# Performance work log

Measured on AMD Instinct MI355X. Metric: run time of the kernel, lower is better.

Reference implementation:

```python
import jax, jax.numpy as jnp
import numpy as np

B, S, D_IN, H = 64, 512, 2, 512


def lstm_cell(x, h, c, Wih, Whh, b):
    # PyTorch nn.LSTM gate layout: [i, f, g, o] stacked along rows of W (4H x in)
    gates = x @ Wih.T + h @ Whh.T + b  # [B, 4H]
    i, f, g, o = jnp.split(gates, 4, axis=-1)
    c = jax.nn.sigmoid(f) * c + jax.nn.sigmoid(i) * jnp.tanh(g)
    h = jax.nn.sigmoid(o) * jnp.tanh(c)
    return h, c


def setup_inputs() -> dict:
    key = jax.random.key(0)
    ks = jax.random.split(key, 12)
    s = 1.0 / np.sqrt(H)  # torch default uniform init scale
    u = lambda k, shape: jax.random.uniform(k, shape, jnp.float32, -s, s)
    return {
        "inputs": jax.random.normal(ks[0], (B, S, D_IN), jnp.float32),
        "enc_Wih": u(ks[1], (4 * H, D_IN)),
        "enc_Whh": u(ks[2], (4 * H, H)),
        "enc_bih": u(ks[3], (4 * H,)),
        "enc_bhh": u(ks[4], (4 * H,)),
        "dec_Wih": u(ks[5], (4 * H, H)),
        "dec_Whh": u(ks[6], (4 * H, H)),
        "dec_bih": u(ks[7], (4 * H,)),
        "dec_bhh": u(ks[8], (4 * H,)),
        "W_key": u(ks[9], (H, H)),
        "W_query": u(ks[10], (H, H)),
        "v": u(ks[11], (H,)),
        "max_output_len": S,
    }


def reference(inputs, enc_Wih, enc_Whh, enc_bih, enc_bhh,
              dec_Wih, dec_Whh, dec_bih, dec_bhh,
              W_key, W_query, v, max_output_len):
    batch, seq_len, _ = inputs.shape
    hid = W_key.shape[0]
    dtype = inputs.dtype

    # ---- Encoder LSTM over the sequence ----
    enc_b = enc_bih + enc_bhh
    h0 = jnp.zeros((batch, hid), dtype)

    def enc_step(carry, x_t):
        h, c = carry
        h, c = lstm_cell(x_t, h, c, enc_Wih, enc_Whh, enc_b)
        return (h, c), h

    (h, c), enc_outs = jax.lax.scan(enc_step, (h0, h0), jnp.swapaxes(inputs, 0, 1))
    enc_outs = jnp.swapaxes(enc_outs, 0, 1)  # [B, S, H]

    # keys are recomputed each step in the torch code but are step-invariant
    keys = enc_outs @ W_key.T  # [B, S, H]
    dec_b = dec_bih + dec_bhh

    # ---- Decoder loop with Bahdanau pointer attention ----
    def dec_step(carry, _):
        h_d, c_d, x = carry
        h_d, c_d = lstm_cell(x, h_d, c_d, dec_Wih, dec_Whh, dec_b)
        query = h_d @ W_query.T                                # [B, H]
        scores = jnp.tanh(query[:, None, :] + keys) @ v        # [B, S]
        probs = jax.nn.softmax(scores, axis=-1)
        context = jnp.einsum('bs,bsh->bh', probs, enc_outs)    # [B, H]
        return (h_d, c_d, context), scores

    x0 = jnp.zeros((batch, hid), dtype)
    _, all_scores = jax.lax.scan(dec_step, (h, c, x0), None, length=max_output_len)
    return jnp.swapaxes(all_scores, 0, 1)  # [B, T, S]
```

## Files before the change

kernel.cpp:

```cpp
#include <hip/hip_runtime.h>

constexpr int kNB = 64;
constexpr int kNS = 512;
constexpr int kNH = 512;
constexpr int kNG = 2048;
constexpr int kNT = 512;

typedef _Float16 chpn_f16;

__device__ __forceinline__ float chpn_sigmoid(float x) {
    return 1.0f / (1.0f + __expf(-x));
}
__device__ __forceinline__ float chpn_tanh(float x) {
    x = fmaxf(fminf(x, 15.0f), -15.0f);
    float e = __expf(2.0f * x);
    return (e - 1.0f) / (e + 1.0f);
}

__global__ void ConvexHullPointerNetwork_57303453663418_kernel(
    const float* ebih, const float* ebhh,
    const float* dbih, const float* dbhh,
    float* enc_b, float* dec_b, float* h0c)
{
    int i = blockIdx.x * 256 + threadIdx.x;
    if (i < kNG) { enc_b[i] = ebih[i] + ebhh[i]; dec_b[i] = dbih[i] + dbhh[i]; }
    if (i < 2 * kNB * kNH) h0c[i] = 0.0f;
}

__global__ __launch_bounds__(256) void chpn_enc_cell(
    const float* __restrict__ inputs, const float* __restrict__ wih,
    const float* __restrict__ whh, const float* __restrict__ bias,
    const float* __restrict__ h_src, float* __restrict__ h_dst,
    float* __restrict__ c_st, chpn_f16* __restrict__ enc_outs, int t)
{
    __shared__ float tile[64][65];
    __shared__ float gate_lds[4][64];
    const int tid = threadIdx.x;
    const int bb = tid & 63, gg = tid >> 6;
    const int j = (int)blockIdx.x;
    const int r = gg * kNH + j;
    const float* w = whh + (size_t)r * kNH;
    float acc = 0.f;
    for (int ch = 0; ch < 8; ++ch) {
        const int k0 = ch * 64;
        for (int i = 0; i < 16; ++i) {
            int e = tid + i * 256; int kk = e & 63, b2 = e >> 6;
            tile[kk][b2] = h_src[b2 * kNH + k0 + kk];
        }
        __syncthreads();
        #pragma unroll
        for (int kk = 0; kk < 64; ++kk)
            acc = fmaf(tile[kk][bb], w[k0 + kk], acc);
        __syncthreads();
    }
    float x0 = inputs[(bb * kNS + t) * 2 + 0];
    float x1 = inputs[(bb * kNS + t) * 2 + 1];
    acc += bias[r] + wih[r * 2] * x0 + wih[r * 2 + 1] * x1;
    gate_lds[gg][bb] = acc;
    __syncthreads();
    if (tid < 64) {
        float gi = gate_lds[0][tid], gf = gate_lds[1][tid];
        float gc = gate_lds[2][tid], go = gate_lds[3][tid];
        float cc = chpn_sigmoid(gf) * c_st[tid * kNH + j] + chpn_sigmoid(gi) * chpn_tanh(gc);
        float hh = chpn_sigmoid(go) * chpn_tanh(cc);
        c_st[tid * kNH + j] = cc;
        h_dst[tid * kNH + j] = hh;
        enc_outs[((size_t)tid * kNS + t) * kNH + j] = (chpn_f16)hh;
    }
}

__global__ __launch_bounds__(256) void chpn_keys_gemm(
    const chpn_f16* __restrict__ enc_outs, const float* __restrict__ wk,
    chpn_f16* __restrict__ keysT)
{
    int bid = blockIdx.x;
    int bb = bid >> 6, ht = (bid >> 3) & 7, st = bid & 7;
    __shared__ float asb[32][66];
    __shared__ float bsb[32][66];
    int tid = threadIdx.x;
    int tx = tid & 15, ty = tid >> 4;
    float acc[4][4] = {};
    for (int j0 = 0; j0 < kNH; j0 += 32) {
        for (int i = 0; i < 8; ++i) {
            int e = tid + i * 256;
            int j = e & 31, s = e >> 5;
            asb[j][s] = (float)enc_outs[((size_t)bb * kNS + st * 64 + s) * kNH + j0 + j];
            bsb[j][s] = wk[(size_t)(ht * 64 + s) * kNH + j0 + j];
        }
        __syncthreads();
        #pragma unroll 8
        for (int j = 0; j < 32; ++j) {
            float a0 = asb[j][tx*4], a1 = asb[j][tx*4+1], a2 = asb[j][tx*4+2], a3 = asb[j][tx*4+3];
            float b0 = bsb[j][ty*4], b1 = bsb[j][ty*4+1], b2 = bsb[j][ty*4+2], b3 = bsb[j][ty*4+3];
            acc[0][0] = fmaf(b0,a0,acc[0][0]); acc[0][1] = fmaf(b0,a1,acc[0][1]);
            acc[0][2] = fmaf(b0,a2,acc[0][2]); acc[0][3] = fmaf(b0,a3,acc[0][3]);
            acc[1][0] = fmaf(b1,a0,acc[1][0]); acc[1][1] = fmaf(b1,a1,acc[1][1]);
            acc[1][2] = fmaf(b1,a2,acc[1][2]); acc[1][3] = fmaf(b1,a3,acc[1][3]);
            acc[2][0] = fmaf(b2,a0,acc[2][0]); acc[2][1] = fmaf(b2,a1,acc[2][1]);
            acc[2][2] = fmaf(b2,a2,acc[2][2]); acc[2][3] = fmaf(b2,a3,acc[2][3]);
            acc[3][0] = fmaf(b3,a0,acc[3][0]); acc[3][1] = fmaf(b3,a1,acc[3][1]);
            acc[3][2] = fmaf(b3,a2,acc[3][2]); acc[3][3] = fmaf(b3,a3,acc[3][3]);
        }
        __syncthreads();
    }
    for (int i = 0; i < 4; ++i)
        for (int k = 0; k < 4; ++k)
            keysT[((size_t)bb * kNH + ht * 64 + ty * 4 + i) * kNS + st * 64 + tx * 4 + k] =
                (chpn_f16)acc[i][k];
}

__global__ __launch_bounds__(256) void chpn_dec_cell(
    const float* __restrict__ wih, const float* __restrict__ whh,
    const float* __restrict__ bias,
    const float* __restrict__ h_src, float* __restrict__ h_dst,
    float* __restrict__ c_st,
    const float* __restrict__ ctx_num, const float* __restrict__ denom,
    int first)
{
    __shared__ float tile[64][65];
    __shared__ float gate_lds[4][64];
    __shared__ float invd[64];
    const int tid = threadIdx.x;
    const int bb = tid & 63, gg = tid >> 6;
    const int j = (int)blockIdx.x;
    if (tid < 64) invd[tid] = first ? 0.0f : (1.0f / denom[tid]);
    __syncthreads();
    const int r = gg * kNH + j;
    float acc = 0.f;
    {
        const float* w = wih + (size_t)r * kNH;
        for (int ch = 0; ch < 8; ++ch) {
            const int k0 = ch * 64;
            for (int i = 0; i < 16; ++i) {
                int e = tid + i * 256; int kk = e & 63, b2 = e >> 6;
                tile[kk][b2] = first ? 0.0f : ctx_num[b2 * kNH + k0 + kk] * invd[b2];
            }
            __syncthreads();
            #pragma unroll
            for (int kk = 0; kk < 64; ++kk)
                acc = fmaf(tile[kk][bb], w[k0 + kk], acc);
            __syncthreads();
        }
    }
    {
        const float* w = whh + (size_t)r * kNH;
        for (int ch = 0; ch < 8; ++ch) {
            const int k0 = ch * 64;
            for (int i = 0; i < 16; ++i) {
                int e = tid + i * 256; int kk = e & 63, b2 = e >> 6;
                tile[kk][b2] = h_src[b2 * kNH + k0 + kk];
            }
            __syncthreads();
            #pragma unroll
            for (int kk = 0; kk < 64; ++kk)
                acc = fmaf(tile[kk][bb], w[k0 + kk], acc);
            __syncthreads();
        }
    }
    acc += bias[r];
    gate_lds[gg][bb] = acc;
    __syncthreads();
    if (tid < 64) {
        float gi = gate_lds[0][tid], gf = gate_lds[1][tid];
        float gc = gate_lds[2][tid], go = gate_lds[3][tid];
        float cc = chpn_sigmoid(gf) * c_st[tid * kNH + j] + chpn_sigmoid(gi) * chpn_tanh(gc);
        float hh = chpn_sigmoid(go) * chpn_tanh(cc);
        c_st[tid * kNH + j] = cc;
        h_dst[tid * kNH + j] = hh;
    }
}

__global__ __launch_bounds__(256) void chpn_query_ws(
    const float* __restrict__ wq, const float* __restrict__ h_src,
    float* __restrict__ query, float* __restrict__ ctx_num,
    float* __restrict__ denom)
{
    __shared__ float tile[128][65];
    __shared__ float qp[4][2][64];
    const int tid = threadIdx.x;
    const int bb = tid & 63, p = tid >> 6;
    const int h0 = (int)blockIdx.x * 2;
    const float* w0 = wq + (size_t)h0 * kNH;
    const float* w1 = w0 + kNH;

    float a0 = 0.f, a1 = 0.f;
    for (int ch = 0; ch < 4; ++ch) {
        const int j0 = ch * 128;
        for (int i = 0; i < 32; ++i) {
            int e = tid + i * 256; int jj = e & 127, b2 = e >> 7;
            tile[jj][b2] = h_src[b2 * kNH + j0 + jj];
        }
        __syncthreads();
        if (ch == p) {
            #pragma unroll 4
            for (int jj = 0; jj < 128; ++jj) {
                float hv = tile[jj][bb];
                a0 = fmaf(hv, w0[j0 + jj], a0);
                a1 = fmaf(hv, w1[j0 + jj], a1);
            }
        }
        __syncthreads();
    }
    qp[p][0][bb] = a0;
    qp[p][1][bb] = a1;
    __syncthreads();
    if (tid < 128) {
        int b2 = tid & 63, hh = tid >> 6;
        float q = qp[0][hh][b2] + qp[1][hh][b2] + qp[2][hh][b2] + qp[3][hh][b2];
        query[b2 * kNH + h0 + hh] = q;
        ctx_num[b2 * kNH + h0 + hh] = 0.0f;
        if (blockIdx.x == 0 && hh == 0) denom[b2] = 0.0f;
    }
}

__global__ __launch_bounds__(1024) void chpn_score_ctx(
    const chpn_f16* __restrict__ keysT, const chpn_f16* __restrict__ enc_outs,
    const float* __restrict__ query, const float* __restrict__ vvec,
    float* __restrict__ ctx_num, float* __restrict__ denom,
    float* __restrict__ out, int t)
{
    __shared__ float ql[kNH], vl[kNH];
    __shared__ float part[16][64];
    __shared__ float el[64];
    int bid = blockIdx.x;
    int bb = bid >> 3, sc = bid & 7;
    int s0 = sc * 64;
    int tid = threadIdx.x;
    int s = tid & 63, hq = tid >> 6;
    if (tid < kNH) { ql[tid] = query[bb * kNH + tid]; vl[tid] = vvec[tid]; }
    __syncthreads();
    float acc = 0.f;
    const chpn_f16* kp = keysT + (size_t)bb * kNH * kNS + s0 + s;
    const int h0 = hq * 32;
    #pragma unroll 4
    for (int h = h0; h < h0 + 32; ++h) {
        float kv = (float)kp[(size_t)h * kNS];
        acc = fmaf(vl[h], chpn_tanh(ql[h] + kv), acc);
    }
    part[hq][s] = acc;
    __syncthreads();
    if (tid < 64) {
        float scv = 0.f;
        #pragma unroll
        for (int q = 0; q < 16; ++q) scv += part[q][tid];
        out[((size_t)bb * kNT + t) * kNS + s0 + tid] = scv;
        float e = __expf(scv);
        el[tid] = e;
        float wsum = e;
        #pragma unroll
        for (int off = 32; off > 0; off >>= 1) wsum += __shfl_down(wsum, off);
        if (tid == 0) atomicAdd(&denom[bb], wsum);
    }
    __syncthreads();
    int j = tid & 511, sh = tid >> 9;
    float a = 0.f;
    const chpn_f16* ep = enc_outs + ((size_t)bb * kNS + s0 + sh * 32) * kNH + j;
    #pragma unroll 4
    for (int ss = 0; ss < 32; ++ss)
        a = fmaf(el[sh * 32 + ss], (float)ep[(size_t)ss * kNH], a);
    atomicAdd(&ctx_num[bb * kNH + j], a);
}

extern "C" void kernel_launch(void* const* d_in, const int* in_sizes, int n_in,
                              void* d_out, int out_size, void* d_ws, size_t ws_size,
                              hipStream_t stream) {
    const float* inputs = (const float*)d_in[0];
    const float* e_wih  = (const float*)d_in[1];
    const float* e_whh  = (const float*)d_in[2];
    const float* e_bih  = (const float*)d_in[3];
    const float* e_bhh  = (const float*)d_in[4];
    const float* d_wih  = (const float*)d_in[5];
    const float* d_whh  = (const float*)d_in[6];
    const float* d_bih  = (const float*)d_in[7];
    const float* d_bhh  = (const float*)d_in[8];
    const float* w_key  = (const float*)d_in[9];
    const float* w_qry  = (const float*)d_in[10];
    const float* v_vec  = (const float*)d_in[11];
    float* out = (float*)d_out;

    float* wsf   = (float*)d_ws;
    float* h0    = wsf;
    float* cst   = h0 + kNB * kNH;
    float* h1    = cst + kNB * kNH;
    float* query = h1 + kNB * kNH;
    float* ctxn  = query + kNB * kNH;
    float* denom = ctxn + kNB * kNH;
    float* encb  = denom + 64;
    float* decb  = encb + kNG;
    chpn_f16* keysH = (chpn_f16*)(decb + kNG);
    chpn_f16* encH  = keysH + (size_t)kNB * kNH * kNS;

    ConvexHullPointerNetwork_57303453663418_kernel<<<256, 256, 0, stream>>>(
        e_bih, e_bhh, d_bih, d_bhh, encb, decb, h0);

    for (int t = 0; t < kNS; ++t) {
        float* hs = (t & 1) ? h1 : h0;
        float* hd = (t & 1) ? h0 : h1;
        chpn_enc_cell<<<512, 256, 0, stream>>>(inputs, e_wih, e_whh, encb,
                                               hs, hd, cst, encH, t);
    }

    chpn_keys_gemm<<<4096, 256, 0, stream>>>(encH, w_key, keysH);

    for (int t = 0; t < kNT; ++t) {
        float* hs = (t & 1) ? h1 : h0;
        float* hd = (t & 1) ? h0 : h1;
        chpn_dec_cell<<<512, 256, 0, stream>>>(d_wih, d_whh, decb,
                                               hs, hd, cst,
                                               ctxn, denom, t == 0 ? 1 : 0);
        chpn_query_ws<<<256, 256, 0, stream>>>(w_qry, hd, query, ctxn, denom);
        chpn_score_ctx<<<512, 1024, 0, stream>>>(keysH, encH, query, v_vec,
                                                 ctxn, denom, out, t);
    }
}
```

Before: 73.68 ms.

## Replace per-step kernel launches with persistent cooperative encoder and decoder kernels

Encoder and decoder each become a single persistent cooperative launch of 256 blocks. Each batch element is handled by a group of 4 blocks that synchronise through atomic spin barriers in global memory instead of through per-timestep kernel launches. Weights are pre-transposed once so that gate, query and context matvecs read them coalesced, and the softmax denominator now uses per-block partial sums. This removes roughly 2000 launches and their launch overhead, but it relies on every block being co-resident and on spin barriers, and a fallback to the old per-step path remains if the cooperative launch fails.

Result: slower. 200.8 ms (+172.5%).

```diff
diff --git a/kernel.cpp b/kernel.cpp
--- a/kernel.cpp
+++ b/kernel.cpp
@@ -1,4 +1,5 @@
 #include <hip/hip_runtime.h>
+#include <hip/hip_cooperative_groups.h>
 
 constexpr int kNB = 64;
 constexpr int kNS = 512;
@@ -17,17 +18,286 @@
     return (e - 1.0f) / (e + 1.0f);
 }
 
+#define CHPN_BAR(barp, nbar)                                        \
+    do {                                                            \
+        __syncthreads();                                            \
+        ++(nbar);                                                   \
+        if (threadIdx.x == 0) {                                     \
+            __threadfence();                                        \
+            atomicAdd((barp), 1);                                   \
+            while (atomicAdd((barp), 0) < 4 * (nbar)) {}            \
+        }                                                           \
+        __syncthreads();                                            \
+        __threadfence();                                            \
+    } while (0)
+
 __global__ void ConvexHullPointerNetwork_57303453663418_kernel(
     const float* ebih, const float* ebhh,
     const float* dbih, const float* dbhh,
-    float* enc_b, float* dec_b, float* h0c)
-{
-    int i = blockIdx.x * 256 + threadIdx.x;
-    if (i < kNG) { enc_b[i] = ebih[i] + ebhh[i]; dec_b[i] = dbih[i] + dbhh[i]; }
-    if (i < 2 * kNB * kNH) h0c[i] = 0.0f;
-}
-
-__global__ __launch_bounds__(256) void chpn_enc_cell(
+    const float* ewhh, const float* dwih, const float* dwhh, const float* wq,
+    float* enc_b, float* dec_b, float* weT, float* wdT, float* wqT,
+    float* h_g, float* cfin, int* bars)
+{
+    size_t i = (size_t)blockIdx.x * 256 + threadIdx.x;
+    size_t stride = (size_t)gridDim.x * 256;
+    for (size_t x = i; x < (size_t)kNG; x += stride) {
+        enc_b[x] = ebih[x] + ebhh[x];
+        dec_b[x] = dbih[x] + dbhh[x];
+    }
+    for (size_t x = i; x < (size_t)kNH * kNG; x += stride) {
+        size_t k = x / kNG, r = x % kNG;
+        weT[x] = ewhh[r * kNH + k];
+    }
+    for (size_t x = i; x < (size_t)2 * kNH * kNG; x += stride) {
+        size_t k = x / kNG, r = x % kNG;
+        wdT[x] = (k < kNH) ? dwih[r * kNH + k] : dwhh[r * kNH + (k - kNH)];
+    }
+    for (size_t x = i; x < (size_t)kNH * kNH; x += stride) {
+        size_t j = x / kNH, h = x % kNH;
+        wqT[x] = wq[h * kNH + j];
+    }
+    for (size_t x = i; x < (size_t)2 * kNB * kNH; x += stride) h_g[x] = 0.0f;
+    for (size_t x = i; x < (size_t)kNB * kNH; x += stride) cfin[x] = 0.0f;
+    for (size_t x = i; x < 2048; x += stride) bars[x] = 0;
+}
+
+__global__ __launch_bounds__(1024) void chpn_enc_p(
+    const float* __restrict__ inputs, const float* __restrict__ wih,
+    const float* __restrict__ weT, const float* __restrict__ bias,
+    float* __restrict__ h_g, float* __restrict__ cfin,
+    chpn_f16* __restrict__ enc_outs, int* __restrict__ bars)
+{
+    __shared__ float xl[kNH];
+    __shared__ float gpart[2][512];
+    __shared__ float gates[4][128];
+    __shared__ float c_l[128];
+    const int tid = threadIdx.x;
+    const int g = (int)blockIdx.x >> 2, q = (int)blockIdx.x & 3;
+    const int j0 = q * 128;
+    const int row = tid & 511, kh = tid >> 9;
+    const int seg = row >> 7, jj = row & 127;
+    const int r = seg * kNH + j0 + jj;
+    const float bias_r = bias[r];
+    const float wx0 = wih[r * 2], wx1 = wih[r * 2 + 1];
+    int* barp = bars + g * 16;
+    int nbar = 0;
+    if (tid < 128) c_l[tid] = 0.0f;
+
+    for (int t = 0; t < kNS; ++t) {
+        const int bufr = t & 1, bufw = bufr ^ 1;
+        if (tid < kNH)
+            xl[tid] = (t == 0) ? 0.0f : h_g[(size_t)bufr * kNB * kNH + g * kNH + tid];
+        __syncthreads();
+        float acc = 0.f;
+        const float* wp = weT + (size_t)(kh * 256) * kNG + r;
+        #pragma unroll 4
+        for (int k = 0; k < 256; ++k)
+            acc = fmaf(wp[(size_t)k * kNG], xl[kh * 256 + k], acc);
+        gpart[kh][row] = acc;
+        __syncthreads();
+        if (tid < 512) {
+            float x0 = inputs[(g * kNS + t) * 2 + 0];
+            float x1 = inputs[(g * kNS + t) * 2 + 1];
+            gates[seg][jj] = gpart[0][tid] + gpart[1][tid] + bias_r +
+                             wx0 * x0 + wx1 * x1;
+        }
+        __syncthreads();
+        if (tid < 128) {
+            float gi = gates[0][tid], gf = gates[1][tid];
+            float gc = gates[2][tid], go = gates[3][tid];
+            float cc = chpn_sigmoid(gf) * c_l[tid] +
+                       chpn_sigmoid(gi) * chpn_tanh(gc);
+            float hh = chpn_sigmoid(go) * chpn_tanh(cc);
+            c_l[tid] = cc;
+            h_g[(size_t)bufw * kNB * kNH + g * kNH + j0 + tid] = hh;
+            enc_outs[((size_t)g * kNS + t) * kNH + j0 + tid] = (chpn_f16)hh;
+        }
+        CHPN_BAR(barp, nbar);
+    }
+    if (tid < 128) cfin[g * kNH + j0 + tid] = c_l[tid];
+}
+
+__global__ __launch_bounds__(256) void chpn_keys_gemm(
+    const chpn_f16* __restrict__ enc_outs, const float* __restrict__ wk,
+    chpn_f16* __restrict__ keysT)
+{
+    int bid = blockIdx.x;
+    int bb = bid >> 6, ht = (bid >> 3) & 7, st = bid & 7;
+    __shared__ float asb[32][66];
+    __shared__ float bsb[32][66];
+    int tid = threadIdx.x;
+    int tx = tid & 15, ty = tid >> 4;
+    float acc[4][4] = {};
+    for (int j0 = 0; j0 < kNH; j0 += 32) {
+        for (int i = 0; i < 8; ++i) {
+            int e = tid + i * 256;
+            int j = e & 31, s = e >> 5;
+            asb[j][s] = (float)enc_outs[((size_t)bb * kNS + st * 64 + s) * kNH + j0 + j];
+            bsb[j][s] = wk[(size_t)(ht * 64 + s) * kNH + j0 + j];
+        }
+        __syncthreads();
+        #pragma unroll 8
+        for (int j = 0; j < 32; ++j) {
+            float a0 = asb[j][tx*4], a1 = asb[j][tx*4+1], a2 = asb[j][tx*4+2], a3 = asb[j][tx*4+3];
+            float b0 = bsb[j][ty*4], b1 = bsb[j][ty*4+1], b2 = bsb[j][ty*4+2], b3 = bsb[j][ty*4+3];
+            acc[0][0] = fmaf(b0,a0,acc[0][0]); acc[0][1] = fmaf(b0,a1,acc[0][1]);
+            acc[0][2] = fmaf(b0,a2,acc[0][2]); acc[0][3] = fmaf(b0,a3,acc[0][3]);
+            acc[1][0] = fmaf(b1,a0,acc[1][0]); acc[1][1] = fmaf(b1,a1,acc[1][1]);
+            acc[1][2] = fmaf(b1,a2,acc[1][2]); acc[1][3] = fmaf(b1,a3,acc[1][3]);
+            acc[2][0] = fmaf(b2,a0,acc[2][0]); acc[2][1] = fmaf(b2,a1,acc[2][1]);
+            acc[2][2] = fmaf(b2,a2,acc[2][2]); acc[2][3] = fmaf(b2,a3,acc[2][3]);
+            acc[3][0] = fmaf(b3,a0,acc[3][0]); acc[3][1] = fmaf(b3,a1,acc[3][1]);
+            acc[3][2] = fmaf(b3,a2,acc[3][2]); acc[3][3] = fmaf(b3,a3,acc[3][3]);
+        }
+        __syncthreads();
+    }
+    for (int i = 0; i < 4; ++i)
+        for (int k = 0; k < 4; ++k)
+            keysT[((size_t)bb * kNH + ht * 64 + ty * 4 + i) * kNS + st * 64 + tx * 4 + k] =
+                (chpn_f16)acc[i][k];
+}
+
+__global__ __launch_bounds__(1024) void chpn_dec_p(
+    const float* __restrict__ wdT, const float* __restrict__ bias,
+    const float* __restrict__ wqT, const float* __restrict__ vvec,
+    const chpn_f16* __restrict__ keysT, const chpn_f16* __restrict__ enc_outs,
+    float* __restrict__ h_g, const float* __restrict__ cfin,
+    float* __restrict__ ctx_g, float* __restrict__ q_g,
+    float* __restrict__ el_g, float* __restrict__ denomp,
+    int* __restrict__ bars, float* __restrict__ out)
+{
+    __shared__ float xl[2 * kNH];
+    __shared__ float gpart[2][512];
+    __shared__ float gates[4][128];
+    __shared__ float c_l[128];
+    __shared__ float vl[kNH];
+    __shared__ float buf8[8][128];
+    __shared__ float dp2[2];
+    __shared__ float dinv_l;
+    const int tid = threadIdx.x;
+    const int g = (int)blockIdx.x >> 2, q = (int)blockIdx.x & 3;
+    const int j0 = q * 128;
+    const int s0 = q * 128;
+    const int h0q = q * 128;
+    const int row = tid & 511, kh = tid >> 9;
+    const int seg = row >> 7, jj = row & 127;
+    const int r = seg * kNH + j0 + jj;
+    const float bias_r = bias[r];
+    int* barp = bars + 1024 + g * 16;
+    int nbar = 0;
+    const chpn_f16* keyb = keysT + (size_t)g * kNH * kNS;
+    const chpn_f16* encb2 = enc_outs + (size_t)g * kNS * kNH;
+
+    if (tid < 128) c_l[tid] = cfin[g * kNH + j0 + tid];
+    if (tid < kNH) vl[tid] = vvec[tid];
+
+    for (int t = 0; t < kNT; ++t) {
+        const int bufr = t & 1, bufw = bufr ^ 1;
+
+        if (tid < kNH)
+            xl[tid] = (t == 0) ? 0.0f : ctx_g[g * kNH + tid];
+        else
+            xl[tid] = h_g[(size_t)bufr * kNB * kNH + g * kNH + (tid - kNH)];
+        __syncthreads();
+        float acc = 0.f;
+        const float* wp = wdT + (size_t)(kh * 512) * kNG + r;
+        #pragma unroll 4
+        for (int k = 0; k < 512; ++k)
+            acc = fmaf(wp[(size_t)k * kNG], xl[kh * 512 + k], acc);
+        gpart[kh][row] = acc;
+        __syncthreads();
+        if (tid < 512) gates[seg][jj] = gpart[0][tid] + gpart[1][tid] + bias_r;
+        __syncthreads();
+        if (tid < 128) {
+            float gi = gates[0][tid], gf = gates[1][tid];
+            float gc = gates[2][tid], go = gates[3][tid];
+            float cc = chpn_sigmoid(gf) * c_l[tid] +
+                       chpn_sigmoid(gi) * chpn_tanh(gc);
+            float hh = chpn_sigmoid(go) * chpn_tanh(cc);
+            c_l[tid] = cc;
+            h_g[(size_t)bufw * kNB * kNH + g * kNH + j0 + tid] = hh;
+        }
+        CHPN_BAR(barp, nbar);
+
+        if (tid < kNH)
+            xl[tid] = h_g[(size_t)bufw * kNB * kNH + g * kNH + tid];
+        __syncthreads();
+        {
+            int hi = tid & 127, js = tid >> 7;
+            float qa = 0.f;
+            #pragma unroll 4
+            for (int j = js * 64; j < js * 64 + 64; ++j)
+                qa = fmaf(xl[j], wqT[(size_t)j * kNH + h0q + hi], qa);
+            buf8[js][hi] = qa;
+        }
+        __syncthreads();
+        if (tid < 128) {
+            float qv = 0.f;
+            #pragma unroll
+            for (int o = 0; o < 8; ++o) qv += buf8[o][tid];
+            q_g[g * kNH + h0q + tid] = qv;
+        }
+        CHPN_BAR(barp, nbar);
+
+        if (tid < kNH) xl[tid] = q_g[g * kNH + tid];
+        __syncthreads();
+        {
+            int si = tid & 127, hs = tid >> 7;
+            float sa = 0.f;
+            const chpn_f16* kp = keyb + s0 + si;
+            #pragma unroll 4
+            for (int h = hs * 64; h < hs * 64 + 64; ++h) {
+                float kv = (float)kp[(size_t)h * kNS];
+                sa = fmaf(vl[h], chpn_tanh(xl[h] + kv), sa);
+            }
+            buf8[hs][si] = sa;
+        }
+        __syncthreads();
+        if (tid < 128) {
+            float scv = 0.f;
+            #pragma unroll
+            for (int o = 0; o < 8; ++o) scv += buf8[o][tid];
+            out[((size_t)g * kNT + t) * kNS + s0 + tid] = scv;
+            float e = __expf(scv);
+            el_g[g * kNH + s0 + tid] = e;
+            float wsum = e;
+            #pragma unroll
+            for (int off = 32; off > 0; off >>= 1)
+                wsum += __shfl_down(wsum, off);
+            if ((tid & 63) == 0) dp2[tid >> 6] = wsum;
+        }
+        __syncthreads();
+        if (tid == 0) denomp[g * 4 + q] = dp2[0] + dp2[1];
+        CHPN_BAR(barp, nbar);
+
+        if (tid < kNH) xl[tid] = el_g[g * kNH + tid];
+        if (tid == 0) {
+            float d = denomp[g * 4] + denomp[g * 4 + 1] +
+                      denomp[g * 4 + 2] + denomp[g * 4 + 3];
+            dinv_l = 1.0f / d;
+        }
+        __syncthreads();
+        {
+            int ji = tid & 127, ss = tid >> 7;
+            float ca = 0.f;
+            const chpn_f16* ep = encb2 + (size_t)(ss * 64) * kNH + j0 + ji;
+            #pragma unroll 4
+            for (int sx = 0; sx < 64; ++sx)
+                ca = fmaf(xl[ss * 64 + sx], (float)ep[(size_t)sx * kNH], ca);
+            buf8[ss][ji] = ca;
+        }
+        __syncthreads();
+        if (tid < 128) {
+            float cv = 0.f;
+            #pragma unroll
+            for (int o = 0; o < 8; ++o) cv += buf8[o][tid];
+            ctx_g[g * kNH + j0 + tid] = cv * dinv_l;
+        }
+        if (t < kNT - 1) CHPN_BAR(barp, nbar);
+    }
+}
+
+__global__ __launch_bounds__(256) void fb_enc_cell(
     const float* __restrict__ inputs, const float* __restrict__ wih,
     const float* __restrict__ whh, const float* __restrict__ bias,
     const float* __restrict__ h_src, float* __restrict__ h_dst,
@@ -69,47 +339,7 @@
     }
 }
 
-__global__ __launch_bounds__(256) void chpn_keys_gemm(
-    const chpn_f16* __restrict__ enc_outs, const float* __restrict__ wk,
-    chpn_f16* __restrict__ keysT)
-{
-    int bid = blockIdx.x;
-    int bb = bid >> 6, ht = (bid >> 3) & 7, st = bid & 7;
-    __shared__ float asb[32][66];
-    __shared__ float bsb[32][66];
-    int tid = threadIdx.x;
-    int tx = tid & 15, ty = tid >> 4;
-    float acc[4][4] = {};
-    for (int j0 = 0; j0 < kNH; j0 += 32) {
-        for (int i = 0; i < 8; ++i) {
-            int e = tid + i * 256;
-            int j = e & 31, s = e >> 5;
-            asb[j][s] = (float)enc_outs[((size_t)bb * kNS + st * 64 + s) * kNH + j0 + j];
-            bsb[j][s] = wk[(size_t)(ht * 64 + s) * kNH + j0 + j];
-        }
-        __syncthreads();
-        #pragma unroll 8
-        for (int j = 0; j < 32; ++j) {
-            float a0 = asb[j][tx*4], a1 = asb[j][tx*4+1], a2 = asb[j][tx*4+2], a3 = asb[j][tx*4+3];
-            float b0 = bsb[j][ty*4], b1 = bsb[j][ty*4+1], b2 = bsb[j][ty*4+2], b3 = bsb[j][ty*4+3];
-            acc[0][0] = fmaf(b0,a0,acc[0][0]); acc[0][1] = fmaf(b0,a1,acc[0][1]);
-            acc[0][2] = fmaf(b0,a2,acc[0][2]); acc[0][3] = fmaf(b0,a3,acc[0][3]);
-            acc[1][0] = fmaf(b1,a0,acc[1][0]); acc[1][1] = fmaf(b1,a1,acc[1][1]);
-            acc[1][2] = fmaf(b1,a2,acc[1][2]); acc[1][3] = fmaf(b1,a3,acc[1][3]);
-            acc[2][0] = fmaf(b2,a0,acc[2][0]); acc[2][1] = fmaf(b2,a1,acc[2][1]);
-            acc[2][2] = fmaf(b2,a2,acc[2][2]); acc[2][3] = fmaf(b2,a3,acc[2][3]);
-            acc[3][0] = fmaf(b3,a0,acc[3][0]); acc[3][1] = fmaf(b3,a1,acc[3][1]);
-            acc[3][2] = fmaf(b3,a2,acc[3][2]); acc[3][3] = fmaf(b3,a3,acc[3][3]);
-        }
-        __syncthreads();
-    }
-    for (int i = 0; i < 4; ++i)
-        for (int k = 0; k < 4; ++k)
-            keysT[((size_t)bb * kNH + ht * 64 + ty * 4 + i) * kNS + st * 64 + tx * 4 + k] =
-                (chpn_f16)acc[i][k];
-}
-
-__global__ __launch_bounds__(256) void chpn_dec_cell(
+__global__ __launch_bounds__(256) void fb_dec_cell(
     const float* __restrict__ wih, const float* __restrict__ whh,
     const float* __restrict__ bias,
     const float* __restrict__ h_src, float* __restrict__ h_dst,
@@ -170,7 +400,7 @@
     }
 }
 
-__global__ __launch_bounds__(256) void chpn_query_ws(
+__global__ __launch_bounds__(256) void fb_query(
     const float* __restrict__ wq, const float* __restrict__ h_src,
     float* __restrict__ query, float* __restrict__ ctx_num,
     float* __restrict__ denom)
@@ -182,7 +412,6 @@
     const int h0 = (int)blockIdx.x * 2;
     const float* w0 = wq + (size_t)h0 * kNH;
     const float* w1 = w0 + kNH;
-
     float a0 = 0.f, a1 = 0.f;
     for (int ch = 0; ch < 4; ++ch) {
         const int j0 = ch * 128;
@@ -206,14 +435,14 @@
     __syncthreads();
     if (tid < 128) {
         int b2 = tid & 63, hh = tid >> 6;
-        float q = qp[0][hh][b2] + qp[1][hh][b2] + qp[2][hh][b2] + qp[3][hh][b2];
-        query[b2 * kNH + h0 + hh] = q;
+        float qv = qp[0][hh][b2] + qp[1][hh][b2] + qp[2][hh][b2] + qp[3][hh][b2];
+        query[b2 * kNH + h0 + hh] = qv;
         ctx_num[b2 * kNH + h0 + hh] = 0.0f;
         if (blockIdx.x == 0 && hh == 0) denom[b2] = 0.0f;
     }
 }
 
-__global__ __launch_bounds__(1024) void chpn_score_ctx(
+__global__ __launch_bounds__(1024) void fb_score_ctx(
     const chpn_f16* __restrict__ keysT, const chpn_f16* __restrict__ enc_outs,
     const float* __restrict__ query, const float* __restrict__ vvec,
     float* __restrict__ ctx_num, float* __restrict__ denom,
@@ -242,7 +471,7 @@
     if (tid < 64) {
         float scv = 0.f;
         #pragma unroll
-        for (int q = 0; q < 16; ++q) scv += part[q][tid];
+        for (int qq = 0; qq < 16; ++qq) scv += part[qq][tid];
         out[((size_t)bb * kNT + t) * kNS + s0 + tid] = scv;
         float e = __expf(scv);
         el[tid] = e;
@@ -279,37 +508,74 @@
     float* out = (float*)d_out;
 
     float* wsf   = (float*)d_ws;
-    float* h0    = wsf;
-    float* cst   = h0 + kNB * kNH;
-    float* h1    = cst + kNB * kNH;
-    float* query = h1 + kNB * kNH;
-    float* ctxn  = query + kNB * kNH;
-    float* denom = ctxn + kNB * kNH;
-    float* encb  = denom + 64;
+    float* encb  = wsf;
     float* decb  = encb + kNG;
-    chpn_f16* keysH = (chpn_f16*)(decb + kNG);
+    float* wqT   = decb + kNG;
+    float* weT   = wqT + (size_t)kNH * kNH;
+    float* wdT   = weT + (size_t)kNH * kNG;
+    float* h_g   = wdT + (size_t)2 * kNH * kNG;
+    float* cfin  = h_g + (size_t)2 * kNB * kNH;
+    float* ctx_g = cfin + (size_t)kNB * kNH;
+    float* q_g   = ctx_g + (size_t)kNB * kNH;
+    float* el_g  = q_g + (size_t)kNB * kNH;
+    float* denomp = el_g + (size_t)kNB * kNH;
+    int*   bars  = (int*)(denomp + 256);
+    chpn_f16* keysH = (chpn_f16*)(bars + 2048);
     chpn_f16* encH  = keysH + (size_t)kNB * kNH * kNS;
 
-    ConvexHullPointerNetwork_57303453663418_kernel<<<256, 256, 0, stream>>>(
-        e_bih, e_bhh, d_bih, d_bhh, encb, decb, h0);
-
-    for (int t = 0; t < kNS; ++t) {
-        float* hs = (t & 1) ? h1 : h0;
-        float* hd = (t & 1) ? h0 : h1;
-        chpn_enc_cell<<<512, 256, 0, stream>>>(inputs, e_wih, e_whh, encb,
-                                               hs, hd, cst, encH, t);
+    ConvexHullPointerNetwork_57303453663418_kernel<<<4096, 256, 0, stream>>>(
+        e_bih, e_bhh, d_bih, d_bhh, e_whh, d_wih, d_whh, w_qry,
+        encb, decb, weT, wdT, wqT, h_g, cfin, bars);
+
+    float* h0 = h_g;
+    float* h1 = h_g + (size_t)kNB * kNH;
+
+    {
+        const float* a0 = inputs; const float* a1 = e_wih;
+        const float* a2 = weT; const float* a3 = encb;
+        float* a4 = h_g; float* a5 = cfin;
+        chpn_f16* a6 = encH; int* a7 = bars;
+        void* args[] = { &a0, &a1, &a2, &a3, &a4, &a5, &a6, &a7 };
+        hipError_t rc = hipLaunchCooperativeKernel((const void*)chpn_enc_p,
+                                                   dim3(256), dim3(1024),
+                                                   args, 0, stream);
+        if (rc != hipSuccess) {
+            (void)hipGetLastError();
+            for (int t = 0; t < kNS; ++t) {
+                float* hs = (t & 1) ? h1 : h0;
+                float* hd = (t & 1) ? h0 : h1;
+                fb_enc_cell<<<512, 256, 0, stream>>>(inputs, e_wih, e_whh, encb,
+                                                     hs, hd, cfin, encH, t);
+            }
+        }
     }
 
     chpn_keys_gemm<<<4096, 256, 0, stream>>>(encH, w_key, keysH);
 
-    for (int t = 0; t < kNT; ++t) {
-        float* hs = (t & 1) ? h1 : h0;
-        float* hd = (t & 1) ? h0 : h1;
-        chpn_dec_cell<<<512, 256, 0, stream>>>(d_wih, d_whh, decb,
-                                               hs, hd, cst,
-                                               ctxn, denom, t == 0 ? 1 : 0);
-        chpn_query_ws<<<256, 256, 0, stream>>>(w_qry, hd, query, ctxn, denom);
-        chpn_score_ctx<<<512, 1024, 0, stream>>>(keysH, encH, query, v_vec,
-                                                 ctxn, denom, out, t);
-    }
-}
+    {
+        const float* a0 = wdT; const float* a1 = decb;
+        const float* a2 = wqT; const float* a3 = v_vec;
+        const chpn_f16* a4 = keysH; const chpn_f16* a5 = encH;
+        float* a6 = h_g; const float* a7 = cfin;
+        float* a8 = ctx_g; float* a9 = q_g; float* a10 = el_g;
+        float* a11 = denomp; int* a12 = bars; float* a13 = out;
+        void* args[] = { &a0, &a1, &a2, &a3, &a4, &a5, &a6, &a7,
+                         &a8, &a9, &a10, &a11, &a12, &a13 };
+        hipError_t rc = hipLaunchCooperativeKernel((const void*)chpn_dec_p,
+                                                   dim3(256), dim3(1024),
+                                                   args, 0, stream);
+        if (rc != hipSuccess) {
+            (void)hipGetLastError();
+            for (int t = 0; t < kNT; ++t) {
+                float* hs = (t & 1) ? h1 : h0;
+                float* hd = (t & 1) ? h0 : h1;
+                fb_dec_cell<<<512, 256, 0, stream>>>(d_wih, d_whh, decb,
+                                                     hs, hd, cfin,
+                                                     ctx_g, denomp, t == 0 ? 1 : 0);
+                fb_query<<<256, 256, 0, stream>>>(w_qry, hd, q_g, ctx_g, denomp);
+                fb_score_ctx<<<512, 1024, 0, stream>>>(keysH, encH, q_g, v_vec,
+                                                       ctx_g, denomp, out, t);
+            }
+        }
+    }
+}
```
